# Optimization experiments

Measured on AMD Instinct MI355X. Metric: run time of the kernel, lower is better.

The kernel has to match this reference:

```python
import jax, jax.numpy as jnp
import numpy as np

RAW_NOISE_STD = 0.1
FAR_DIST = 1e10


def setup_inputs() -> dict:
    key = jax.random.key(0)
    k1, k2, k3 = jax.random.split(key, 3)
    B, C, Z, Y, X = 1, 32, 64, 256, 256
    feat = jax.random.normal(k1, (B, C, Z, Y, X), dtype=jnp.float32)
    occ = jax.random.normal(k2, (B, 1, Z, Y, X), dtype=jnp.float32)
    z_dist = jnp.arange(Z, dtype=jnp.float32) * 0.5  # increasing integration times
    noise = jax.random.normal(k3, (B * Y * X, Z), dtype=jnp.float32)
    return {"feat": feat, "occ": occ, "z_dist": z_dist, "noise": noise}


def reference(feat, occ, z_dist, noise):
    B, C, Z, Y, X = feat.shape
    N = B * Y * X  # rays
    # [B,C,Z,Y,X] -> [N, Z, C] ; occ [B,1,Z,Y,X] -> [N, Z]
    feat_r = jnp.transpose(feat, (0, 3, 4, 2, 1)).reshape(N, Z, C)
    occ_r = jnp.transpose(occ, (0, 3, 4, 2, 1)).reshape(N, Z)
    z_vals = jnp.broadcast_to(z_dist.reshape(1, Z), (N, Z))

    # dists between samples, last one ~infinite
    dists = z_vals[:, 1:] - z_vals[:, :-1]
    dists = jnp.concatenate([dists, jnp.full((N, 1), FAR_DIST, dists.dtype)], axis=1)

    alpha = 1.0 - jnp.exp(-jax.nn.relu(occ_r + noise * RAW_NOISE_STD) * dists)
    trans = jnp.cumprod(1.0 - alpha + 1e-10, axis=-1)
    weights = alpha * jnp.concatenate(
        [jnp.ones((N, 1), alpha.dtype), trans[:, :-1]], axis=1
    )  # [N, Z]

    # weights are detached for the feature composite (matches torch .detach())
    feat_map = jnp.sum(jax.lax.stop_gradient(weights)[..., None] * feat_r, axis=-2)  # [N,C]
    acc_map = jnp.clip(jnp.sum(weights, axis=-1), 0.0, 1.0)  # [N]

    feat_e = jnp.transpose(feat_map.reshape(B, Y, X, C), (0, 3, 1, 2))  # [B,C,Y,X]
    acc_e = jnp.transpose(acc_map.reshape(B, Y, X, 1), (0, 3, 1, 2))    # [B,1,Y,X]
    rgb_e = jax.nn.sigmoid(feat_e) - 0.5
    total_loss = jnp.zeros((), dtype=jnp.float32)
    return (total_loss, rgb_e, feat_e, acc_e)
```

## Files before the change

kernel.cpp:

```cpp
#include <hip/hip_runtime.h>
#include <stdint.h>

#define ZS 64
#define CS 32
#define YX 65536
#define RPB 64
#define FAR_DIST 1e10f
#define NOISE_LD 65

__global__ __launch_bounds__(256) void rendernet_kernel(
    const float* __restrict__ feat,
    const float* __restrict__ occ,
    const float* __restrict__ zd,
    const float* __restrict__ noise,
    float* __restrict__ out)
{
    __shared__ float w_lds[ZS * RPB];
    __shared__ float noise_lds[RPB * NOISE_LD];
    __shared__ float dist_s[ZS];

    const int t  = threadIdx.x;
    const int r0 = blockIdx.x * RPB;

    const float4* ng = reinterpret_cast<const float4*>(noise + (size_t)r0 * ZS);
    #pragma unroll
    for (int j = 0; j < 4; ++j) {
        int idx = j * 256 + t;
        float4 v = ng[idx];
        int ray = idx >> 4;
        int zb  = (idx & 15) * 4;
        float* p = &noise_lds[ray * NOISE_LD + zb];
        p[0] = v.x; p[1] = v.y; p[2] = v.z; p[3] = v.w;
    }
    if (t < ZS) {
        float a = zd[t];
        dist_s[t] = (t < ZS - 1) ? (zd[t + 1] - a) : FAR_DIST;
    }
    __syncthreads();

    if (t < RPB) {
        const int n = r0 + t;
        float T = 1.0f, wsum = 0.0f;
        #pragma unroll
        for (int z = 0; z < ZS; ++z) {
            float o   = occ[(size_t)z * YX + n];
            float ns  = noise_lds[t * NOISE_LD + z];
            float raw = fmaxf(o + ns * 0.1f, 0.0f);
            float alpha = 1.0f - __expf(-raw * dist_s[z]);
            float w = alpha * T;
            w_lds[z * RPB + t] = w;
            wsum += w;
            T *= (1.0f - alpha + 1e-10f);
        }
        out[(size_t)1 + 2u * (size_t)CS * YX + n] = fminf(fmaxf(wsum, 0.0f), 1.0f);
        if (blockIdx.x == 0 && t == 0) out[0] = 0.0f;
    }
    __syncthreads();

    const int ray = t & 63;
    const int g   = t >> 6;
    const int n   = r0 + ray;
    const float* fb = feat + (size_t)(g * 8) * ZS * YX + n;

    float acc[8];
    #pragma unroll
    for (int j = 0; j < 8; ++j) acc[j] = 0.0f;

    #pragma unroll 4
    for (int z = 0; z < ZS; ++z) {
        float w = w_lds[z * RPB + ray];
        #pragma unroll
        for (int j = 0; j < 8; ++j)
            acc[j] += w * fb[((size_t)j * ZS + z) * YX];
    }

    float* rgb = out + 1;
    float* fe  = out + 1 + (size_t)CS * YX;
    #pragma unroll
    for (int j = 0; j < 8; ++j) {
        const size_t o = (size_t)(g * 8 + j) * YX + n;
        fe[o]  = acc[j];
        rgb[o] = 1.0f / (1.0f + __expf(-acc[j])) - 0.5f;
    }
}

extern "C" void kernel_launch(void* const* d_in, const int* in_sizes, int n_in,
                              void* d_out, int out_size, void* d_ws, size_t ws_size,
                              hipStream_t stream) {
    const float* feat  = (const float*)d_in[0];
    const float* occ   = (const float*)d_in[1];
    const float* zdist = (const float*)d_in[2];
    const float* noise = (const float*)d_in[3];
    float* out = (float*)d_out;

    rendernet_kernel<<<YX / RPB, 256, 0, stream>>>(feat, occ, zdist, noise, out);
}
```

Baseline: 721.8 us.

## Vectorize feature loads as float4 and drop LDS noise staging

Each thread now accumulates four adjacent rays for four channels using float4 loads of feat and float4 reads of the weight tile. Rays per block rise to 128, with a launch-bounds occupancy hint of two blocks. The noise tile is no longer staged through shared memory: each ray thread reads its own noise row directly as float4. The aim is wider, fewer global memory transactions on the dominant feature stream. In exchange the grid has half as many blocks, and the output stores become per-element writes with a 16-byte stride between lanes.

New measurement: 718.7 us. About the same (-0.4%).

```diff
diff --git a/kernel.cpp b/kernel.cpp
--- a/kernel.cpp
+++ b/kernel.cpp
@@ -4,11 +4,11 @@
 #define ZS 64
 #define CS 32
 #define YX 65536
-#define RPB 64
+#define YX4 16384
+#define RPB 128
 #define FAR_DIST 1e10f
-#define NOISE_LD 65
 
-__global__ __launch_bounds__(256) void rendernet_kernel(
+__global__ __launch_bounds__(256, 2) void rendernet_kernel(
     const float* __restrict__ feat,
     const float* __restrict__ occ,
     const float* __restrict__ zd,
@@ -16,22 +16,11 @@
     float* __restrict__ out)
 {
     __shared__ float w_lds[ZS * RPB];
-    __shared__ float noise_lds[RPB * NOISE_LD];
     __shared__ float dist_s[ZS];
 
     const int t  = threadIdx.x;
     const int r0 = blockIdx.x * RPB;
 
-    const float4* ng = reinterpret_cast<const float4*>(noise + (size_t)r0 * ZS);
-    #pragma unroll
-    for (int j = 0; j < 4; ++j) {
-        int idx = j * 256 + t;
-        float4 v = ng[idx];
-        int ray = idx >> 4;
-        int zb  = (idx & 15) * 4;
-        float* p = &noise_lds[ray * NOISE_LD + zb];
-        p[0] = v.x; p[1] = v.y; p[2] = v.z; p[3] = v.w;
-    }
     if (t < ZS) {
         float a = zd[t];
         dist_s[t] = (t < ZS - 1) ? (zd[t + 1] - a) : FAR_DIST;
@@ -40,47 +29,66 @@
 
     if (t < RPB) {
         const int n = r0 + t;
+        const float4* nz4 = reinterpret_cast<const float4*>(noise + (size_t)n * ZS);
         float T = 1.0f, wsum = 0.0f;
-        #pragma unroll
-        for (int z = 0; z < ZS; ++z) {
-            float o   = occ[(size_t)z * YX + n];
-            float ns  = noise_lds[t * NOISE_LD + z];
-            float raw = fmaxf(o + ns * 0.1f, 0.0f);
-            float alpha = 1.0f - __expf(-raw * dist_s[z]);
-            float w = alpha * T;
-            w_lds[z * RPB + t] = w;
-            wsum += w;
-            T *= (1.0f - alpha + 1e-10f);
+        #pragma unroll 4
+        for (int zq = 0; zq < ZS / 4; ++zq) {
+            float4 nv = nz4[zq];
+            float nsv[4] = {nv.x, nv.y, nv.z, nv.w};
+            #pragma unroll
+            for (int dz = 0; dz < 4; ++dz) {
+                const int z = zq * 4 + dz;
+                float o     = occ[(size_t)z * YX + n];
+                float raw   = fmaxf(o + nsv[dz] * 0.1f, 0.0f);
+                float alpha = 1.0f - __expf(-raw * dist_s[z]);
+                float w     = alpha * T;
+                w_lds[z * RPB + t] = w;
+                wsum += w;
+                T *= (1.0f - alpha + 1e-10f);
+            }
         }
         out[(size_t)1 + 2u * (size_t)CS * YX + n] = fminf(fmaxf(wsum, 0.0f), 1.0f);
         if (blockIdx.x == 0 && t == 0) out[0] = 0.0f;
     }
     __syncthreads();
 
-    const int ray = t & 63;
-    const int g   = t >> 6;
-    const int n   = r0 + ray;
-    const float* fb = feat + (size_t)(g * 8) * ZS * YX + n;
+    const int q  = t & 31;
+    const int g  = t >> 5;
+    const int n0 = r0 + q * 4;
 
-    float acc[8];
+    const float4* f4 = reinterpret_cast<const float4*>(feat);
+    const size_t base4 = (size_t)(g * 4) * ZS * YX4 + (size_t)(n0 >> 2);
+
+    float4 acc[4];
     #pragma unroll
-    for (int j = 0; j < 8; ++j) acc[j] = 0.0f;
+    for (int j = 0; j < 4; ++j) acc[j] = make_float4(0.f, 0.f, 0.f, 0.f);
 
     #pragma unroll 4
     for (int z = 0; z < ZS; ++z) {
-        float w = w_lds[z * RPB + ray];
+        const float4 w = *reinterpret_cast<const float4*>(&w_lds[z * RPB + (q << 2)]);
         #pragma unroll
-        for (int j = 0; j < 8; ++j)
-            acc[j] += w * fb[((size_t)j * ZS + z) * YX];
+        for (int j = 0; j < 4; ++j) {
+            const float4 f = f4[base4 + (size_t)(j * ZS + z) * YX4];
+            acc[j].x += w.x * f.x;
+            acc[j].y += w.y * f.y;
+            acc[j].z += w.z * f.z;
+            acc[j].w += w.w * f.w;
+        }
     }
 
     float* rgb = out + 1;
     float* fe  = out + 1 + (size_t)CS * YX;
     #pragma unroll
-    for (int j = 0; j < 8; ++j) {
-        const size_t o = (size_t)(g * 8 + j) * YX + n;
-        fe[o]  = acc[j];
-        rgb[o] = 1.0f / (1.0f + __expf(-acc[j])) - 0.5f;
+    for (int j = 0; j < 4; ++j) {
+        const int c = g * 4 + j;
+        const float va[4] = {acc[j].x, acc[j].y, acc[j].z, acc[j].w};
+        #pragma unroll
+        for (int k = 0; k < 4; ++k) {
+            const size_t o = (size_t)c * YX + (size_t)(n0 + k);
+            const float v = va[k];
+            fe[o]  = v;
+            rgb[o] = 1.0f / (1.0f + __expf(-v)) - 0.5f;
+        }
     }
 }
 
```
